# Performance work log

Hardware: AMD Instinct MI355X
Metric: run time of the kernel (lower is better)

Reference implementation:

```python
import jax, jax.numpy as jnp
import numpy as np

N_NODES = 50000
N_EDGES = 800000
VOCAB = 10000
EMB = 128
HID = 128
OUT = 128
N_GRAPHS = 512


def setup_inputs() -> dict:
    key = jax.random.key(0)
    ks = jax.random.split(key, 12)
    edge_index = jax.random.randint(ks[0], (2, N_EDGES), 0, N_NODES, dtype=jnp.int64 if jax.config.jax_enable_x64 else jnp.int32)
    features = jax.random.randint(ks[1], (N_NODES, 1), 0, VOCAB, dtype=jnp.int32)
    batch = jnp.sort(jax.random.randint(ks[2], (N_NODES,), 0, N_GRAPHS, dtype=jnp.int32))
    s = 0.02
    emb = jax.random.normal(ks[3], (VOCAB, EMB), dtype=jnp.float32) * s
    W1 = jax.random.normal(ks[4], (EMB, HID), dtype=jnp.float32) * (1.0 / np.sqrt(EMB))
    b1 = jnp.zeros((HID,), dtype=jnp.float32)
    W2 = jax.random.normal(ks[5], (HID, HID), dtype=jnp.float32) * (1.0 / np.sqrt(HID))
    b2 = jnp.zeros((HID,), dtype=jnp.float32)
    W3 = jax.random.normal(ks[6], (HID, OUT), dtype=jnp.float32) * (1.0 / np.sqrt(HID))
    b3 = jnp.zeros((OUT,), dtype=jnp.float32)
    fcW = jax.random.normal(ks[7], (OUT, 1), dtype=jnp.float32) * (1.0 / np.sqrt(OUT))
    fcb = jnp.zeros((1,), dtype=jnp.float32)
    return dict(edge_index=edge_index, features=features, batch=batch,
                emb=emb, W1=W1, b1=b1, W2=W2, b2=b2, W3=W3, b3=b3,
                fcW=fcW, fcb=fcb)


def _gcn_conv(x, W, b, src, dst):
    # PyG GCNConv: add self-loops, symmetric deg^{-1/2} normalization,
    # linear transform first (no bias), then normalized scatter-add, then + bias.
    x = x @ W                                                    # [N, F_out]
    deg = jax.ops.segment_sum(jnp.ones((src.shape[0],), x.dtype), dst,
                              num_segments=N_NODES) + 1.0        # +1 self-loop
    dinv = jax.lax.rsqrt(deg)                                    # [N]
    norm = dinv[src] * dinv[dst]                                 # [E]
    msg = x[src] * norm[:, None]                                 # [E, F_out] gather
    agg = jax.ops.segment_sum(msg, dst, num_segments=N_NODES)    # scatter-add
    agg = agg + x * (dinv * dinv)[:, None]                       # self-loop term
    return agg + b


def reference(edge_index, features, batch, emb, W1, b1, W2, b2, W3, b3, fcW, fcb):
    src, dst = edge_index[0], edge_index[1]
    x = emb[features[:, 0]]                                      # [N, EMB]
    x = jax.nn.relu(_gcn_conv(x, W1, b1, src, dst))
    x = jax.nn.relu(_gcn_conv(x, W2, b2, src, dst))
    x = jax.nn.relu(_gcn_conv(x, W3, b3, src, dst))
    # global mean pool over graphs
    sums = jax.ops.segment_sum(x, batch, num_segments=N_GRAPHS)  # [G, OUT]
    cnts = jax.ops.segment_sum(jnp.ones((N_NODES,), x.dtype), batch,
                               num_segments=N_GRAPHS)
    pooled = sums / jnp.maximum(cnts, 1.0)[:, None]
    return (pooled @ fcW + fcb)[:, 0]                            # [G]
```

## Files before the change

kernel.cpp:

```cpp
#include <hip/hip_runtime.h>
#include <hip/hip_fp16.h>

#define N_NODES 50000
#define N_EDGES 800000
#define N_GRAPHS 512
#define VOCAB 10000
#define C 128
#define NBUCK 196
#define A_BLOCKS 200
#define EDGES_PER_A (N_EDGES / A_BLOCKS)
#define SE_CAP 8192

typedef __attribute__((ext_vector_type(8))) short short8v;
typedef __attribute__((ext_vector_type(4))) float f32x4;

__device__ __forceinline__ unsigned short f2bf(float f){
  unsigned u = __builtin_bit_cast(unsigned, f);
  unsigned r = u + 0x7FFFu + ((u >> 16) & 1u);
  return (unsigned short)(r >> 16);
}
__device__ __forceinline__ float bf2f(unsigned short h){
  unsigned u = ((unsigned)h) << 16;
  return __builtin_bit_cast(float, u);
}
__device__ __forceinline__ float h2f(short s){
  return __half2float(__builtin_bit_cast(__half, (unsigned short)s));
}

__global__ __launch_bounds__(256) void k_pre(const int* __restrict__ dst, int* __restrict__ blockHist,
                      const int* __restrict__ batch, int* __restrict__ gStart,
                      const float* __restrict__ W1, const float* __restrict__ W2,
                      const float* __restrict__ W3, short* __restrict__ Bp,
                      const float* __restrict__ emb, __half* __restrict__ embh){
  __shared__ int h[256];
  int b = blockIdx.x, t = threadIdx.x;
  if (b < A_BLOCKS){
    h[t] = 0; __syncthreads();
    int base = b * EDGES_PER_A;
    for (int i = t; i < EDGES_PER_A; i += 256)
      atomicAdd(&h[dst[base+i] >> 8], 1);
    __syncthreads();
    blockHist[t*A_BLOCKS + b] = h[t];
  } else if (b < A_BLOCKS+NBUCK){
    int i = (b-A_BLOCKS)*256 + t;
    if (i >= N_NODES) return;
    int bb = batch[i];
    int pb = (i==0) ? -1 : batch[i-1];
    for (int g=pb+1; g<=bb; g++) gStart[g] = i;
    if (i == N_NODES-1)
      for (int g=bb+1; g<=N_GRAPHS; g++) gStart[g] = N_NODES;
  } else if (b < A_BLOCKS+NBUCK+24){
    int idx = (b-A_BLOCKS-NBUCK)*256 + t;
    int layer = idx / 2048;
    int r = idx - layer*2048;
    const float* W = (layer==0) ? W1 : (layer==1) ? W2 : W3;
    short* Bh = Bp + (size_t)layer*32768;
    short* Bl = Bh + 16384;
    int lane = r & 63, tile = r >> 6;
    int kt = tile >> 3, ct = tile & 7;
    int q = lane >> 4, c = ct*16 + (lane & 15);
    #pragma unroll
    for (int i=0;i<8;i++){
      int k = kt*32 + q*8 + i;
      float w = W[k*C + c];
      unsigned short hh = f2bf(w);
      unsigned short ll = f2bf(w - bf2f(hh));
      Bh[(size_t)(tile*64 + lane)*8 + i] = (short)hh;
      Bl[(size_t)(tile*64 + lane)*8 + i] = (short)ll;
    }
  } else {
    int idx = (b-A_BLOCKS-NBUCK-24)*256 + t;
    const float2* s = (const float2*)emb;
    __half2* d2 = (__half2*)embh;
    for (int i = idx; i < VOCAB*C/2; i += 64*256)
      d2[i] = __float22half2_rn(s[i]);
  }
}

__global__ __launch_bounds__(64) void k_binScanA(const int* __restrict__ blockHist,
                        int* __restrict__ blockOfs, int* __restrict__ bucketTot){
  int b = blockIdx.x;
  int l = threadIdx.x;
  int carry = 0;
  for (int c = 0; c < 256; c += 64){
    int idx = c + l;
    int v = (idx < A_BLOCKS) ? blockHist[b*A_BLOCKS + idx] : 0;
    int x = v;
    #pragma unroll
    for (int off=1; off<64; off<<=1){
      int y = __shfl_up(x, off);
      if (l >= off) x += y;
    }
    if (idx < A_BLOCKS) blockOfs[b*A_BLOCKS + idx] = carry + x - v;
    carry += __shfl(x, 63);
  }
  if (l == 0) bucketTot[b] = carry;
}

__global__ __launch_bounds__(256) void k_binScatter(const int* __restrict__ src, const int* __restrict__ dst,
                           const int* __restrict__ bucketTot, const int* __restrict__ blockOfs,
                           unsigned* __restrict__ binned){
  __shared__ int s[256], ofs[256], cur[256];
  int t = threadIdx.x;
  int tv = bucketTot[t];
  s[t] = tv; __syncthreads();
  for (int off=1; off<256; off<<=1){
    int u = (t>=off) ? s[t-off] : 0;
    __syncthreads();
    s[t] += u;
    __syncthreads();
  }
  ofs[t] = (s[t] - tv) + blockOfs[t*A_BLOCKS + blockIdx.x];
  cur[t] = 0;
  __syncthreads();
  int base = blockIdx.x * EDGES_PER_A;
  for (int i = t; i < EDGES_PER_A; i += 256){
    int d = dst[base+i];
    int b = d >> 8;
    int p = atomicAdd(&cur[b], 1);
    binned[ofs[b] + p] = (unsigned)(src[base+i] & 0xFFFF) | ((unsigned)(d & 0xFF) << 16);
  }
}

__global__ __launch_bounds__(256) void k_binFinal(const unsigned* __restrict__ binned,
                         const int* __restrict__ bucketTot, const int* __restrict__ feat,
                         unsigned short* __restrict__ eSrc, unsigned short* __restrict__ eFeat,
                         int* __restrict__ rowStart, int* __restrict__ deg, float* __restrict__ dinv){
  __shared__ int h[256], pre[256], cur[256], excl[256];
  __shared__ unsigned short sE[SE_CAP];
  int b = blockIdx.x;
  int t = threadIdx.x;
  int tv = bucketTot[t];
  pre[t] = tv; __syncthreads();
  for (int off=1; off<256; off<<=1){
    int u = (t>=off) ? pre[t-off] : 0;
    __syncthreads();
    pre[t] += u;
    __syncthreads();
  }
  excl[t] = pre[t] - tv;
  __syncthreads();
  int base = excl[b], cnt = bucketTot[b];
  int nodeBase = b << 8;
  h[t] = 0; __syncthreads();
  for (int i = t; i < cnt; i += 256)
    atomicAdd(&h[binned[base+i] >> 16], 1);
  __syncthreads();
  pre[t] = h[t]; __syncthreads();
  for (int off=1; off<256; off<<=1){
    int u = (t>=off) ? pre[t-off] : 0;
    __syncthreads();
    pre[t] += u;
    __syncthreads();
  }
  int node = nodeBase + t;
  if (node < N_NODES){
    int d = h[t];
    deg[node] = d;
    rowStart[node] = base + pre[t] - d;
    dinv[node] = rsqrtf((float)d + 1.0f);
  }
  cur[t] = pre[t] - h[t];
  __syncthreads();
  for (int i = t; i < cnt; i += 256){
    unsigned v = binned[base+i];
    int dl = v >> 16;
    int p = atomicAdd(&cur[dl], 1);
    unsigned short s = (unsigned short)(v & 0xFFFF);
    if (p < SE_CAP) sE[p] = s;
    else eSrc[base + p] = s;
  }
  __syncthreads();
  int lim = cnt < SE_CAP ? cnt : SE_CAP;
  for (int i = t; i < lim; i += 256){
    unsigned short sv = sE[i];
    eSrc[base+i]  = sv;
    eFeat[base+i] = (unsigned short)feat[sv];
  }
  for (int i = SE_CAP + t; i < cnt; i += 256){
    eFeat[base+i] = (unsigned short)feat[eSrc[base+i]];
  }
}


template<int LAYER>
__global__ __launch_bounds__(256) void k_layer(
      const __half* __restrict__ gsrc,
      const unsigned short* __restrict__ eSrc, const unsigned short* __restrict__ eFeat,
      const int* __restrict__ rowStart, const int* __restrict__ deg,
      const float* __restrict__ dinv, const int* __restrict__ feat,
      const short* __restrict__ Bh, const short* __restrict__ Bl,
      const float* __restrict__ bias, const float* __restrict__ fcW,
      __half* __restrict__ xsOut, float* __restrict__ dots){
  __shared__ unsigned short uhl[16*C];
  __shared__ unsigned short ull[16*C];
  __shared__ float dotb[16][4];
  int t = threadIdx.x;
  int wave = t>>6, lane = t&63;
  int sub = lane>>4, l16 = lane&15;
  int node0 = blockIdx.x*16;
  int r = wave*4 + sub;
  int node = node0 + r;

  float a[8];
  {
    int rs = rowStart[node], len = deg[node];
    float dn = dinv[node];
    const short8v* X = (const short8v*)gsrc;
    if (LAYER == 1){
      short8v v = X[(size_t)feat[node]*16 + l16];
      #pragma unroll
      for (int i=0;i<8;i++) a[i] = dn * h2f(v[i]);
      int k = 0;
      for (; k+8<=len; k+=8){
        int f[8]; float dd[8];
        #pragma unroll
        for (int j=0;j<8;j++){
          int e = rs+k+j;
          f[j] = eFeat[e];
          dd[j] = dinv[eSrc[e]];
        }
        short8v v8[8];
        #pragma unroll
        for (int j=0;j<8;j++) v8[j] = X[(size_t)f[j]*16 + l16];
        #pragma unroll
        for (int j=0;j<8;j++)
          #pragma unroll
          for (int i=0;i<8;i++) a[i] = fmaf(dd[j], h2f(v8[j][i]), a[i]);
      }
      for (; k<len; k++){
        float dd = dinv[eSrc[rs+k]];
        short8v v1 = X[(size_t)eFeat[rs+k]*16 + l16];
        #pragma unroll
        for (int i=0;i<8;i++) a[i] = fmaf(dd, h2f(v1[i]), a[i]);
      }
    } else {
      short8v v = X[(size_t)node*16 + l16];
      #pragma unroll
      for (int i=0;i<8;i++) a[i] = h2f(v[i]);
      int k = 0;
      for (; k+8<=len; k+=8){
        int s[8];
        #pragma unroll
        for (int j=0;j<8;j++) s[j] = eSrc[rs+k+j];
        short8v v8[8];
        #pragma unroll
        for (int j=0;j<8;j++) v8[j] = X[(size_t)s[j]*16 + l16];
        #pragma unroll
        for (int j=0;j<8;j++)
          #pragma unroll
          for (int i=0;i<8;i++) a[i] += h2f(v8[j][i]);
      }
      for (; k<len; k++){
        short8v v1 = X[(size_t)eSrc[rs+k]*16 + l16];
        #pragma unroll
        for (int i=0;i<8;i++) a[i] += h2f(v1[i]);
      }
    }
    #pragma unroll
    for (int i=0;i<8;i++) a[i] *= dn;
  }
  {
    short8v hv, lv;
    #pragma unroll
    for (int i=0;i<8;i++){
      unsigned short hh = f2bf(a[i]);
      hv[i] = (short)hh;
      lv[i] = (short)f2bf(a[i] - bf2f(hh));
    }
    unsigned boff = (unsigned)(r*256 + l16*16) ^ ((unsigned)(r&7)<<4);
    *(short8v*)((char*)uhl + boff) = hv;
    *(short8v*)((char*)ull + boff) = lv;
  }
  __syncthreads();

  int r15 = lane & 15, q = lane >> 4;
  const short8v* BH = (const short8v*)Bh;
  const short8v* BL = (const short8v*)Bl;
  f32x4 acc[2];
  acc[0] = (f32x4){0.f,0.f,0.f,0.f};
  acc[1] = (f32x4){0.f,0.f,0.f,0.f};
  #pragma unroll
  for (int kt=0; kt<4; kt++){
    unsigned boff = (unsigned)(r15*256 + (kt*4+q)*16) ^ ((unsigned)(r15&7)<<4);
    short8v ah = *(const short8v*)((const char*)uhl + boff);
    short8v al = *(const short8v*)((const char*)ull + boff);
    #pragma unroll
    for (int c=0;c<2;c++){
      int ct = wave*2 + c;
      short8v bh = BH[(kt*8+ct)*64 + lane];
      short8v bl = BL[(kt*8+ct)*64 + lane];
      acc[c] = __builtin_amdgcn_mfma_f32_16x16x32_bf16(ah, bh, acc[c], 0, 0, 0);
      acc[c] = __builtin_amdgcn_mfma_f32_16x16x32_bf16(al, bh, acc[c], 0, 0, 0);
      acc[c] = __builtin_amdgcn_mfma_f32_16x16x32_bf16(ah, bl, acc[c], 0, 0, 0);
    }
  }
  float bb[2] = { bias[(wave*2)*16 + r15], bias[(wave*2+1)*16 + r15] };
  if (LAYER == 3){
    float fw[2] = { fcW[(wave*2)*16 + r15], fcW[(wave*2+1)*16 + r15] };
    #pragma unroll
    for (int j=0;j<4;j++){
      float s = fmaxf(acc[0][j] + bb[0], 0.f)*fw[0]
              + fmaxf(acc[1][j] + bb[1], 0.f)*fw[1];
      s += __shfl_xor(s, 1);
      s += __shfl_xor(s, 2);
      s += __shfl_xor(s, 4);
      s += __shfl_xor(s, 8);
      if (r15 == 0) dotb[q*4 + j][wave] = s;
    }
    __syncthreads();
    if (t < 16) dots[node0 + t] = dotb[t][0] + dotb[t][1] + dotb[t][2] + dotb[t][3];
  } else {
    #pragma unroll
    for (int j=0;j<4;j++){
      int rz = node0 + q*4 + j;
      float d = dinv[rz];
      #pragma unroll
      for (int c=0;c<2;c++){
        float v = fmaxf(acc[c][j] + bb[c], 0.f);
        xsOut[(size_t)rz*C + (wave*2+c)*16 + r15] = __float2half(v * d);
      }
    }
  }
}


__global__ void k_pool_seg(const float* __restrict__ dots, const int* __restrict__ gStart,
                           const float* __restrict__ fcb, float* __restrict__ out){
  __shared__ float s[256];
  int g = blockIdx.x;
  int st = gStart[g], en = gStart[g+1];
  float acc = 0.f;
  for (int i = st + threadIdx.x; i < en; i += 256) acc += dots[i];
  s[threadIdx.x] = acc; __syncthreads();
  for (int off=128; off>0; off>>=1){
    if (threadIdx.x < off) s[threadIdx.x] += s[threadIdx.x+off];
    __syncthreads();
  }
  if (threadIdx.x==0) out[g] = s[0]/fmaxf((float)(en-st),1.0f) + fcb[0];
}


extern "C" void kernel_launch(void* const* d_in, const int* in_sizes, int n_in,
                              void* d_out, int out_size, void* d_ws, size_t ws_size,
                              hipStream_t stream){
  const int* edge  = (const int*)d_in[0];
  const int* srcI  = edge;
  const int* dstI  = edge + N_EDGES;
  const int* feat  = (const int*)d_in[1];
  const int* batch = (const int*)d_in[2];
  const float* emb = (const float*)d_in[3];
  const float* W1  = (const float*)d_in[4];
  const float* b1  = (const float*)d_in[5];
  const float* W2  = (const float*)d_in[6];
  const float* b2  = (const float*)d_in[7];
  const float* W3  = (const float*)d_in[8];
  const float* b3  = (const float*)d_in[9];
  const float* fcW = (const float*)d_in[10];
  const float* fcb = (const float*)d_in[11];
  float* out = (float*)d_out;

  __half* xsA = (__half*)d_ws;
  __half* xsB = xsA + (size_t)N_NODES*C;
  __half* embh = xsB + (size_t)N_NODES*C;
  unsigned* binned = (unsigned*)(embh + (size_t)VOCAB*C);
  unsigned short* eSrc  = (unsigned short*)(binned + N_EDGES);
  unsigned short* eFeat = eSrc + N_EDGES;
  int* rowStart = (int*)(eFeat + N_EDGES);
  int* deg      = rowStart + N_NODES;
  float* dinv   = (float*)(deg + N_NODES);
  int* blockHist = (int*)(dinv + N_NODES);
  int* blockOfs  = blockHist + 256*A_BLOCKS;
  int* bucketTot = blockOfs + 256*A_BLOCKS;
  int* gStart    = bucketTot + 256;
  float* dots   = (float*)(gStart + 520);
  short* Bpack  = (short*)(dots + N_NODES);
  short* Bh1 = Bpack,           * Bl1 = Bpack + 16384;
  short* Bh2 = Bpack + 2*16384, * Bl2 = Bpack + 3*16384;
  short* Bh3 = Bpack + 4*16384, * Bl3 = Bpack + 5*16384;

  k_pre       <<<A_BLOCKS+NBUCK+24+64, 256, 0, stream>>>(dstI, blockHist, batch, gStart,
                                                         W1, W2, W3, Bpack, emb, embh);
  k_binScanA  <<<256, 64, 0, stream>>>(blockHist, blockOfs, bucketTot);
  k_binScatter<<<A_BLOCKS, 256, 0, stream>>>(srcI, dstI, bucketTot, blockOfs, binned);
  k_binFinal  <<<NBUCK, 256, 0, stream>>>(binned, bucketTot, feat, eSrc, eFeat,
                                          rowStart, deg, dinv);

  int LBLOCKS = N_NODES/16;
  k_layer<1><<<LBLOCKS, 256, 0, stream>>>(embh, eSrc, eFeat, rowStart, deg, dinv, feat,
                                          Bh1, Bl1, b1, nullptr, xsB, nullptr);
  k_layer<2><<<LBLOCKS, 256, 0, stream>>>(xsB, eSrc, nullptr, rowStart, deg, dinv, nullptr,
                                          Bh2, Bl2, b2, nullptr, xsA, nullptr);
  k_layer<3><<<LBLOCKS, 256, 0, stream>>>(xsA, eSrc, nullptr, rowStart, deg, dinv, nullptr,
                                          Bh3, Bl3, b3, fcW, nullptr, dots);

  k_pool_seg<<<N_GRAPHS, 256, 0, stream>>>(dots, gStart, fcb, out);
}
```

Before: 168.3 us.

## Prescale layer-1 input per node and software-pipeline the neighbor gather loop

k_binFinal now writes a per-node fp16 tensor xs0 = dinv[node] * emb[feat[node]], so layer 1 becomes a plain unweighted gather over eSrc and the eFeat array and its per-edge dinv lookups disappear. The aggregation loop in k_layer is restructured to double-buffer index and row loads across 8-edge chunks, and the remainder is handled with a fixed 7-wide predicated batch. It also sets launch_bounds occupancy to 4 blocks. Costs are an extra N×C fp16 write/read for xs0, one more rounding of the layer-1 input to fp16, and higher register pressure from the two row buffers.

```diff
diff --git a/kernel.cpp b/kernel.cpp
--- a/kernel.cpp
+++ b/kernel.cpp
@@ -124,9 +124,11 @@
 
 __global__ __launch_bounds__(256) void k_binFinal(const unsigned* __restrict__ binned,
                          const int* __restrict__ bucketTot, const int* __restrict__ feat,
-                         unsigned short* __restrict__ eSrc, unsigned short* __restrict__ eFeat,
+                         const __half* __restrict__ embh,
+                         unsigned short* __restrict__ eSrc, __half* __restrict__ xs0,
                          int* __restrict__ rowStart, int* __restrict__ deg, float* __restrict__ dinv){
   __shared__ int h[256], pre[256], cur[256], excl[256];
+  __shared__ float dinvS[256];
   __shared__ unsigned short sE[SE_CAP];
   int b = blockIdx.x;
   int t = threadIdx.x;
@@ -154,12 +156,15 @@
     __syncthreads();
   }
   int node = nodeBase + t;
+  float dn = 0.f;
   if (node < N_NODES){
     int d = h[t];
     deg[node] = d;
     rowStart[node] = base + pre[t] - d;
-    dinv[node] = rsqrtf((float)d + 1.0f);
-  }
+    dn = rsqrtf((float)d + 1.0f);
+    dinv[node] = dn;
+  }
+  dinvS[t] = dn;
   cur[t] = pre[t] - h[t];
   __syncthreads();
   for (int i = t; i < cnt; i += 256){
@@ -172,23 +177,29 @@
   }
   __syncthreads();
   int lim = cnt < SE_CAP ? cnt : SE_CAP;
-  for (int i = t; i < lim; i += 256){
-    unsigned short sv = sE[i];
-    eSrc[base+i]  = sv;
-    eFeat[base+i] = (unsigned short)feat[sv];
-  }
-  for (int i = SE_CAP + t; i < cnt; i += 256){
-    eFeat[base+i] = (unsigned short)feat[eSrc[base+i]];
+  for (int i = t; i < lim; i += 256) eSrc[base+i] = sE[i];
+  int l16 = t & 15;
+  for (int n = t >> 4; n < 256; n += 16){
+    int nd = nodeBase + n;
+    if (nd < N_NODES){
+      short8v v = ((const short8v*)embh)[(size_t)feat[nd]*16 + l16];
+      float d = dinvS[n];
+      short8v o;
+      #pragma unroll
+      for (int i=0;i<8;i++)
+        o[i] = (short)__builtin_bit_cast(unsigned short, __float2half(d * h2f(v[i])));
+      ((short8v*)xs0)[(size_t)nd*16 + l16] = o;
+    }
   }
 }
 
 
 template<int LAYER>
-__global__ __launch_bounds__(256) void k_layer(
+__global__ __launch_bounds__(256, 4) void k_layer(
       const __half* __restrict__ gsrc,
-      const unsigned short* __restrict__ eSrc, const unsigned short* __restrict__ eFeat,
+      const unsigned short* __restrict__ eSrc,
       const int* __restrict__ rowStart, const int* __restrict__ deg,
-      const float* __restrict__ dinv, const int* __restrict__ feat,
+      const float* __restrict__ dinv,
       const short* __restrict__ Bh, const short* __restrict__ Bl,
       const float* __restrict__ bias, const float* __restrict__ fcW,
       __half* __restrict__ xsOut, float* __restrict__ dots){
@@ -207,54 +218,68 @@
     int rs = rowStart[node], len = deg[node];
     float dn = dinv[node];
     const short8v* X = (const short8v*)gsrc;
-    if (LAYER == 1){
-      short8v v = X[(size_t)feat[node]*16 + l16];
-      #pragma unroll
-      for (int i=0;i<8;i++) a[i] = dn * h2f(v[i]);
-      int k = 0;
-      for (; k+8<=len; k+=8){
-        int f[8]; float dd[8];
-        #pragma unroll
-        for (int j=0;j<8;j++){
-          int e = rs+k+j;
-          f[j] = eFeat[e];
-          dd[j] = dinv[eSrc[e]];
-        }
-        short8v v8[8];
-        #pragma unroll
-        for (int j=0;j<8;j++) v8[j] = X[(size_t)f[j]*16 + l16];
+    short8v sv = X[(size_t)node*16 + l16];
+    #pragma unroll
+    for (int i=0;i<8;i++) a[i] = h2f(sv[i]);
+
+    int nb = len >> 3;
+    int k = nb << 3;
+    if (nb >= 2){
+      int iA[8], iB[8];
+      short8v rA[8], rB[8];
+      #pragma unroll
+      for (int j=0;j<8;j++) iA[j] = eSrc[rs+j];
+      #pragma unroll
+      for (int j=0;j<8;j++) iB[j] = eSrc[rs+8+j];
+      #pragma unroll
+      for (int j=0;j<8;j++) rA[j] = X[(size_t)iA[j]*16 + l16];
+      for (int c=2; c<nb; c++){
+        int iC[8];
+        #pragma unroll
+        for (int j=0;j<8;j++) iC[j] = eSrc[rs + c*8 + j];
+        #pragma unroll
+        for (int j=0;j<8;j++) rB[j] = X[(size_t)iB[j]*16 + l16];
         #pragma unroll
         for (int j=0;j<8;j++)
           #pragma unroll
-          for (int i=0;i<8;i++) a[i] = fmaf(dd[j], h2f(v8[j][i]), a[i]);
+          for (int i=0;i<8;i++) a[i] += h2f(rA[j][i]);
+        #pragma unroll
+        for (int j=0;j<8;j++){ rA[j]=rB[j]; iB[j]=iC[j]; }
       }
-      for (; k<len; k++){
-        float dd = dinv[eSrc[rs+k]];
-        short8v v1 = X[(size_t)eFeat[rs+k]*16 + l16];
-        #pragma unroll
-        for (int i=0;i<8;i++) a[i] = fmaf(dd, h2f(v1[i]), a[i]);
-      }
-    } else {
-      short8v v = X[(size_t)node*16 + l16];
-      #pragma unroll
-      for (int i=0;i<8;i++) a[i] = h2f(v[i]);
-      int k = 0;
-      for (; k+8<=len; k+=8){
-        int s[8];
-        #pragma unroll
-        for (int j=0;j<8;j++) s[j] = eSrc[rs+k+j];
-        short8v v8[8];
-        #pragma unroll
-        for (int j=0;j<8;j++) v8[j] = X[(size_t)s[j]*16 + l16];
-        #pragma unroll
-        for (int j=0;j<8;j++)
+      #pragma unroll
+      for (int j=0;j<8;j++) rB[j] = X[(size_t)iB[j]*16 + l16];
+      #pragma unroll
+      for (int j=0;j<8;j++)
+        #pragma unroll
+        for (int i=0;i<8;i++) a[i] += h2f(rA[j][i]);
+      #pragma unroll
+      for (int j=0;j<8;j++)
+        #pragma unroll
+        for (int i=0;i<8;i++) a[i] += h2f(rB[j][i]);
+    } else if (nb == 1){
+      int s1[8]; short8v v1[8];
+      #pragma unroll
+      for (int j=0;j<8;j++) s1[j] = eSrc[rs+j];
+      #pragma unroll
+      for (int j=0;j<8;j++) v1[j] = X[(size_t)s1[j]*16 + l16];
+      #pragma unroll
+      for (int j=0;j<8;j++)
+        #pragma unroll
+        for (int i=0;i<8;i++) a[i] += h2f(v1[j][i]);
+    }
+    int rem = len - k;
+    if (rem > 0){
+      int sR[7]; short8v vR[7];
+      #pragma unroll
+      for (int j=0;j<7;j++) sR[j] = (j < rem) ? (int)eSrc[rs+k+j] : node;
+      #pragma unroll
+      for (int j=0;j<7;j++) vR[j] = X[(size_t)sR[j]*16 + l16];
+      #pragma unroll
+      for (int j=0;j<7;j++){
+        if (j < rem){
           #pragma unroll
-          for (int i=0;i<8;i++) a[i] += h2f(v8[j][i]);
-      }
-      for (; k<len; k++){
-        short8v v1 = X[(size_t)eSrc[rs+k]*16 + l16];
-        #pragma unroll
-        for (int i=0;i<8;i++) a[i] += h2f(v1[i]);
+          for (int i=0;i<8;i++) a[i] += h2f(vR[j][i]);
+        }
       }
     }
     #pragma unroll
@@ -362,11 +387,11 @@
 
   __half* xsA = (__half*)d_ws;
   __half* xsB = xsA + (size_t)N_NODES*C;
-  __half* embh = xsB + (size_t)N_NODES*C;
+  __half* xs0 = xsB + (size_t)N_NODES*C;
+  __half* embh = xs0 + (size_t)N_NODES*C;
   unsigned* binned = (unsigned*)(embh + (size_t)VOCAB*C);
   unsigned short* eSrc  = (unsigned short*)(binned + N_EDGES);
-  unsigned short* eFeat = eSrc + N_EDGES;
-  int* rowStart = (int*)(eFeat + N_EDGES);
+  int* rowStart = (int*)(eSrc + N_EDGES);
   int* deg      = rowStart + N_NODES;
   float* dinv   = (float*)(deg + N_NODES);
   int* blockHist = (int*)(dinv + N_NODES);
@@ -383,15 +408,15 @@
                                                          W1, W2, W3, Bpack, emb, embh);
   k_binScanA  <<<256, 64, 0, stream>>>(blockHist, blockOfs, bucketTot);
   k_binScatter<<<A_BLOCKS, 256, 0, stream>>>(srcI, dstI, bucketTot, blockOfs, binned);
-  k_binFinal  <<<NBUCK, 256, 0, stream>>>(binned, bucketTot, feat, eSrc, eFeat,
+  k_binFinal  <<<NBUCK, 256, 0, stream>>>(binned, bucketTot, feat, embh, eSrc, xs0,
                                           rowStart, deg, dinv);
 
   int LBLOCKS = N_NODES/16;
-  k_layer<1><<<LBLOCKS, 256, 0, stream>>>(embh, eSrc, eFeat, rowStart, deg, dinv, feat,
+  k_layer<1><<<LBLOCKS, 256, 0, stream>>>(xs0, eSrc, rowStart, deg, dinv,
                                           Bh1, Bl1, b1, nullptr, xsB, nullptr);
-  k_layer<2><<<LBLOCKS, 256, 0, stream>>>(xsB, eSrc, nullptr, rowStart, deg, dinv, nullptr,
+  k_layer<2><<<LBLOCKS, 256, 0, stream>>>(xsB, eSrc, rowStart, deg, dinv,
                                           Bh2, Bl2, b2, nullptr, xsA, nullptr);
-  k_layer<3><<<LBLOCKS, 256, 0, stream>>>(xsA, eSrc, nullptr, rowStart, deg, dinv, nullptr,
+  k_layer<3><<<LBLOCKS, 256, 0, stream>>>(xsA, eSrc, rowStart, deg, dinv,
                                           Bh3, Bl3, b3, fcW, nullptr, dots);
 
   k_pool_seg<<<N_GRAPHS, 256, 0, stream>>>(dots, gStart, fcb, out);
```

Measured after the change: 167.1 us, median of 2. About the same (-0.7%).
